# Kernel optimization log

Hardware: AMD Instinct MI355X
Metric: run time of the kernel (lower is better)

The kernel has to match this reference:

```python
import jax, jax.numpy as jnp
import numpy as np


def _spectral_norm(W, u):
    # W: [out, in] (1x1 conv weight flattened), u: [out]
    # one power-iteration step (torch does this under no_grad), then
    # sigma = u' @ W @ v with gradient flowing through W only.
    v = W.T @ u
    v = v / jnp.linalg.norm(v)
    u2 = W @ v
    u2 = u2 / jnp.linalg.norm(u2)
    v = jax.lax.stop_gradient(v)
    u2 = jax.lax.stop_gradient(u2)
    sigma = u2 @ (W @ v)
    return W / sigma


def setup_inputs() -> dict:
    key = jax.random.key(0)
    ks = jax.random.split(key, 8)
    B, C, H, W = 32, 512, 32, 32
    Cq = C // 8  # 64
    x = jax.random.normal(ks[0], (B, C, H, W), dtype=jnp.float32)
    s = 1.0 / np.sqrt(C)
    return {
        "x": x,
        "Wq": jax.random.normal(ks[1], (Cq, C), dtype=jnp.float32) * s,
        "bq": jnp.zeros((Cq,), dtype=jnp.float32),
        "uq": jax.random.normal(ks[2], (Cq,), dtype=jnp.float32),
        "Wk": jax.random.normal(ks[3], (Cq, C), dtype=jnp.float32) * s,
        "bk": jnp.zeros((Cq,), dtype=jnp.float32),
        "uk": jax.random.normal(ks[4], (Cq,), dtype=jnp.float32),
        "Wv": jax.random.normal(ks[5], (C, C), dtype=jnp.float32) * s,
        "bv": jnp.zeros((C,), dtype=jnp.float32),
        "uv": jax.random.normal(ks[6], (C,), dtype=jnp.float32),
        "gamma": jnp.float32(0.5),
    }


def reference(x, Wq, bq, uq, Wk, bk, uk, Wv, bv, uv, gamma):
    B, C, H, W = x.shape
    N = H * W
    f = x.reshape(B, C, N)                                   # [B,C,N]
    # 1x1 conv == channel matmul with spectral-normalized weights
    q = jnp.einsum('oc,bcn->bno', _spectral_norm(Wq, uq), f) + bq          # [B,N,Cq]
    k = jnp.einsum('oc,bcn->bon', _spectral_norm(Wk, uk), f) + bk[:, None]  # [B,Cq,N]
    v = jnp.einsum('oc,bcn->bon', _spectral_norm(Wv, uv), f) + bv[:, None]  # [B,C,N]
    qk = jnp.einsum('bno,bom->bnm', q, k)                    # [B,N,N], no 1/sqrt(d)
    attn = jax.nn.softmax(qk, axis=1)                        # softmax over QUERY axis (dim 1)
    o = jnp.einsum('bcn,bnm->bcm', v, attn).reshape(B, C, H, W)
    return gamma * o + x
```

## Files before the change

kernel.cpp:

```cpp
#include <hip/hip_runtime.h>
#include <hip/hip_bf16.h>

typedef __hip_bfloat16 bf16;
typedef __bf16 bf16x8 __attribute__((ext_vector_type(8)));
typedef float  f32x4  __attribute__((ext_vector_type(4)));
typedef unsigned short u16x8 __attribute__((ext_vector_type(8)));

#define C_IN  512
#define N_SP  1024
#define BATCH 32

__device__ __forceinline__ float ldmix(const void* p, size_t i, int f32) {
    return f32 ? ((const float*)p)[i] : __bfloat162float(((const bf16*)p)[i]);
}
__device__ __forceinline__ void stmix(void* p, size_t i, float v, int f32) {
    if (f32) ((float*)p)[i] = v;
    else     ((bf16*)p)[i] = __float2bfloat16(v);
}
__device__ __forceinline__ unsigned short bfbits(float f) {
    bf16 t = __float2bfloat16(f);
    return *reinterpret_cast<unsigned short*>(&t);
}
__device__ __forceinline__ float bf2f(unsigned short h) {
    union { unsigned u; float f; } c; c.u = ((unsigned)h) << 16; return c.f;
}
__device__ __forceinline__ void ldvec8(const void* W, size_t base, int f32, float v[8]) {
    if (f32) {
        const float4* p = reinterpret_cast<const float4*>((const float*)W + base);
        float4 a = p[0], b = p[1];
        v[0] = a.x; v[1] = a.y; v[2] = a.z; v[3] = a.w;
        v[4] = b.x; v[5] = b.y; v[6] = b.z; v[7] = b.w;
    } else {
        u16x8 h = *reinterpret_cast<const u16x8*>((const bf16*)W + base);
#pragma unroll
        for (int j = 0; j < 8; ++j) v[j] = bf2f(h[j]);
    }
}

__device__ __forceinline__ void lds_barrier() {
    asm volatile("s_waitcnt lgkmcnt(0)" ::: "memory");
    __builtin_amdgcn_sched_barrier(0);
    __builtin_amdgcn_s_barrier();
    __builtin_amdgcn_sched_barrier(0);
}

__device__ __forceinline__ void tile_decode(int bid, int nblk, int& z, int& mc) {
    int GBk = nblk >> 5;
    if ((GBk & 7) == 0) {
        z  = (bid & 7) + 8 * ((bid >> 3) >> 5);
        mc = (bid >> 3) & 31;
    } else {
        z  = bid >> 5;
        mc = bid & 31;
    }
}

__global__ void k_detect(const unsigned short* __restrict__ xh, int* __restrict__ flag)
{
    __shared__ int red[256];
    int tid = threadIdx.x;
    unsigned short h = xh[2 * tid];
    int e = (h >> 7) & 0xFF;
    red[tid] = (e == 0 || (e >= 96 && e <= 159)) ? 1 : 0;
    __syncthreads();
    for (int s = 128; s > 0; s >>= 1) { if (tid < s) red[tid] += red[tid + s]; __syncthreads(); }
    if (tid == 0) *flag = (red[0] < 192) ? 1 : 0;
}

__global__ __launch_bounds__(256) void k_sn1(
    const void* __restrict__ Wq, const void* __restrict__ uq,
    const void* __restrict__ Wk, const void* __restrict__ uk,
    const void* __restrict__ Wv, const void* __restrict__ uv,
    const int* __restrict__ flag, float* __restrict__ tpart)
{
    __shared__ float sh_u[64];
    __shared__ float sh_acc[4][512];
    int f32 = *flag;
    int bx = blockIdx.x;
    const void *W, *u; int oc, slot;
    if (bx == 0)      { W = Wq; u = uq; oc = 0;      slot = 0; }
    else if (bx == 1) { W = Wk; u = uk; oc = 0;      slot = 1; }
    else              { W = Wv; u = uv; oc = bx - 2; slot = bx; }
    int tid = threadIdx.x, wave = tid >> 6, lane = tid & 63;
    if (tid < 64) sh_u[tid] = ldmix(u, oc * 64 + tid, f32);
    __syncthreads();

    float acc[8];
#pragma unroll
    for (int j = 0; j < 8; ++j) acc[j] = 0.f;
    int obase = oc * 64 + wave * 16;
#pragma unroll 4
    for (int i = 0; i < 16; ++i) {
        int o = obase + i;
        float w8[8]; ldvec8(W, (size_t)o * C_IN + lane * 8, f32, w8);
        float uo = sh_u[o - oc * 64];
#pragma unroll
        for (int j = 0; j < 8; ++j) acc[j] += w8[j] * uo;
    }
#pragma unroll
    for (int j = 0; j < 8; ++j) sh_acc[wave][lane * 8 + j] = acc[j];
    __syncthreads();
    for (int c = tid; c < 512; c += 256)
        tpart[(size_t)slot * 512 + c] =
            sh_acc[0][c] + sh_acc[1][c] + sh_acc[2][c] + sh_acc[3][c];
}

__global__ __launch_bounds__(512) void k_sn2(
    const void* __restrict__ Wq, const void* __restrict__ Wk,
    const void* __restrict__ Wv, const int* __restrict__ flag,
    const float* __restrict__ tpart, float* __restrict__ sig)
{
    __shared__ float sh_t[512];
    __shared__ float red[512];
    int f32 = *flag;
    int m = blockIdx.x;
    const void* W; int out, slot0, nch;
    if (m == 0)      { W = Wq; out = 64;  slot0 = 0; nch = 1; }
    else if (m == 1) { W = Wk; out = 64;  slot0 = 1; nch = 1; }
    else             { W = Wv; out = 512; slot0 = 2; nch = 8; }
    int tid = threadIdx.x, wave = tid >> 6, lane = tid & 63;

    float t = 0.f;
    for (int c2 = 0; c2 < nch; ++c2) t += tpart[(size_t)(slot0 + c2) * 512 + tid];
    sh_t[tid] = t;
    red[tid] = t * t;
    __syncthreads();
    for (int s = 256; s > 0; s >>= 1) { if (tid < s) red[tid] += red[tid + s]; __syncthreads(); }
    float t2 = red[0];
    __syncthreads();

    float tl[8];
#pragma unroll
    for (int j = 0; j < 8; ++j) tl[j] = sh_t[lane * 8 + j];

    float s2 = 0.f;
#pragma unroll 2
    for (int o = wave; o < out; o += 8) {
        float w8[8]; ldvec8(W, (size_t)o * C_IN + lane * 8, f32, w8);
        float d = 0.f;
#pragma unroll
        for (int j = 0; j < 8; ++j) d += w8[j] * tl[j];
#pragma unroll
        for (int off = 32; off > 0; off >>= 1) d += __shfl_xor(d, off);
        if (lane == 0) s2 += d * d;
    }
    __syncthreads();
    red[tid] = (lane == 0) ? s2 : 0.f;
    __syncthreads();
    for (int s = 256; s > 0; s >>= 1) { if (tid < s) red[tid] += red[tid + s]; __syncthreads(); }
    if (tid == 0) sig[m] = sqrtf(t2 / red[0]);
}

__global__ __launch_bounds__(256) void k_wscale(
    const void* __restrict__ Wq, const void* __restrict__ bq,
    const void* __restrict__ Wk, const void* __restrict__ bk,
    const void* __restrict__ Wv, const void* __restrict__ bv,
    const float* __restrict__ sig, const int* __restrict__ flag,
    bf16* __restrict__ Wb, bf16* __restrict__ Wlo, float* __restrict__ biasf)
{
    int f32 = *flag;
    int r = blockIdx.x;
    const void *W, *b; int row; float s;
    if (r < 64)       { W = Wq; b = bq; row = r;       s = sig[0]; }
    else if (r < 128) { W = Wk; b = bk; row = r - 64;  s = sig[1]; }
    else              { W = Wv; b = bv; row = r - 128; s = sig[2]; }
    for (int c = threadIdx.x; c < C_IN; c += 256) {
        float w = ldmix(W, (size_t)row * C_IN + c, f32) * s;
        bf16 hi = __float2bfloat16(w);
        Wb[(size_t)r * C_IN + c] = hi;
        if (r < 128)
            Wlo[(size_t)r * C_IN + c] = __float2bfloat16(w - __bfloat162float(hi));
    }
    if (threadIdx.x == 0) biasf[r] = ldmix(b, row, f32);
}

__global__ __launch_bounds__(256) void k_xt(
    const void* __restrict__ x, const int* __restrict__ flag,
    char* __restrict__ SX, int batch0)
{
    __shared__ float tile[64][65];
    int f32 = *flag;
    int z = blockIdx.z;
    int n0 = blockIdx.x * 64, c0 = blockIdx.y * 64;
    size_t xoff = (size_t)(batch0 + z) * C_IN * N_SP;
    bf16* xTh = (bf16*)(SX + (size_t)z * 4194304);
    bf16* xTl = xTh + 524288;
    int tid = threadIdx.x;
#pragma unroll
    for (int i = 0; i < 4; ++i) {
        int idx = tid + i * 256;
        int c = idx >> 4, nq = idx & 15;
#pragma unroll
        for (int t = 0; t < 4; ++t)
            tile[c][nq * 4 + t] = ldmix(x, xoff + (size_t)(c0 + c) * N_SP + n0 + nq * 4 + t, f32);
    }
    __syncthreads();
#pragma unroll
    for (int i = 0; i < 16; ++i) {
        int idx = tid + i * 256;
        int n = idx >> 6, c = idx & 63;
        float v = tile[c][n];
        bf16 hi = __float2bfloat16(v);
        xTh[(size_t)(n0 + n) * C_IN + c0 + c] = hi;
        xTl[(size_t)(n0 + n) * C_IN + c0 + c] = __float2bfloat16(v - __bfloat162float(hi));
    }
}

__global__ __launch_bounds__(256) void k_qkv_v(
    const bf16* __restrict__ Wb, const float* __restrict__ biasf,
    const char* __restrict__ SX, bf16* __restrict__ YV)
{
    __shared__ __bf16 Als[2][128][40];
    __shared__ __bf16 Bls[2][128][40];
    int z, mc; tile_decode(blockIdx.x, gridDim.x, z, mc);
    int n0 = (mc >> 2) * 128;
    int r0 = 128 + (mc & 3) * 128;
    const bf16* xTh = (const bf16*)(SX + (size_t)z * 4194304);
    bf16* Yv = YV + (size_t)z * 524288;
    int tid = threadIdx.x, wave = tid >> 6, lane = tid & 63, quad = lane >> 4, l16 = lane & 15;
    int wc = (wave >> 1) * 64, wm = (wave & 1) * 64;
    int row0 = tid >> 2, row1 = row0 + 64, ch = tid & 3;

    f32x4 acc[4][4];
#pragma unroll
    for (int i = 0; i < 4; ++i)
#pragma unroll
        for (int j = 0; j < 4; ++j) acc[i][j] = (f32x4){0.f, 0.f, 0.f, 0.f};

    uint4 ra0, ra1, rb0, rb1;
#define LDV(t_) { int k0 = (t_) * 32; \
    ra0 = *reinterpret_cast<const uint4*>(&Wb[(size_t)(r0 + row0) * C_IN + k0 + ch * 8]); \
    ra1 = *reinterpret_cast<const uint4*>(&Wb[(size_t)(r0 + row1) * C_IN + k0 + ch * 8]); \
    rb0 = *reinterpret_cast<const uint4*>(&xTh[(size_t)(n0 + row0) * C_IN + k0 + ch * 8]); \
    rb1 = *reinterpret_cast<const uint4*>(&xTh[(size_t)(n0 + row1) * C_IN + k0 + ch * 8]); }
    LDV(0);
#pragma unroll 2
    for (int t = 0; t < 16; ++t) {
        int cur = t & 1;
        *reinterpret_cast<uint4*>(&Als[cur][row0][ch * 8]) = ra0;
        *reinterpret_cast<uint4*>(&Als[cur][row1][ch * 8]) = ra1;
        *reinterpret_cast<uint4*>(&Bls[cur][row0][ch * 8]) = rb0;
        *reinterpret_cast<uint4*>(&Bls[cur][row1][ch * 8]) = rb1;
        if (t + 1 < 16) LDV(t + 1);
        lds_barrier();
        bf16x8 a[4], b[4];
#pragma unroll
        for (int i = 0; i < 4; ++i)
            a[i] = *reinterpret_cast<const bf16x8*>(&Als[cur][wc + i * 16 + l16][quad * 8]);
#pragma unroll
        for (int j = 0; j < 4; ++j)
            b[j] = *reinterpret_cast<const bf16x8*>(&Bls[cur][wm + j * 16 + l16][quad * 8]);
#pragma unroll
        for (int i = 0; i < 4; ++i)
#pragma unroll
            for (int j = 0; j < 4; ++j)
                acc[i][j] = __builtin_amdgcn_mfma_f32_16x16x32_bf16(a[i], b[j], acc[i][j], 0, 0, 0);
    }
#undef LDV
#pragma unroll
    for (int i = 0; i < 4; ++i)
#pragma unroll
        for (int j = 0; j < 4; ++j)
#pragma unroll
            for (int r = 0; r < 4; ++r) {
                int c = r0 + wc + i * 16 + quad * 4 + r;
                int n = n0 + wm + j * 16 + l16;
                Yv[(size_t)(c - 128) * N_SP + n] = __float2bfloat16(acc[i][j][r] + biasf[c]);
            }
}

__global__ __launch_bounds__(256) void k_qkv_qk(
    const bf16* __restrict__ Wb, const bf16* __restrict__ Wlo,
    const float* __restrict__ biasf, const char* __restrict__ SX,
    bf16* __restrict__ QT, bf16* __restrict__ KT)
{
    __shared__ __bf16 Ah[2][64][40], Al[2][64][40], Bh[2][64][40], Bl[2][64][40];
    int z, mc; tile_decode(blockIdx.x, gridDim.x, z, mc);
    int n0 = (mc >> 1) * 64;
    int m0 = (mc & 1) * 64;
    const bf16* xTh = (const bf16*)(SX + (size_t)z * 4194304);
    const bf16* xTl = xTh + 524288;
    bf16* qt = QT + (size_t)z * 65536;
    bf16* kt = KT + (size_t)z * 65536;
    int tid = threadIdx.x, wave = tid >> 6, lane = tid & 63, quad = lane >> 4, l16 = lane & 15;
    int wmh = (wave >> 1) * 32, wnh = (wave & 1) * 32;
    int row = tid >> 2, ch = tid & 3;

    f32x4 acc[2][2];
#pragma unroll
    for (int i = 0; i < 2; ++i)
#pragma unroll
        for (int j = 0; j < 2; ++j) acc[i][j] = (f32x4){0.f, 0.f, 0.f, 0.f};

    uint4 rah, ral, rbh, rbl;
#define LDQK(t_) { int k0 = (t_) * 32; \
    rah = *reinterpret_cast<const uint4*>(&Wb [(size_t)(m0 + row) * C_IN + k0 + ch * 8]); \
    ral = *reinterpret_cast<const uint4*>(&Wlo[(size_t)(m0 + row) * C_IN + k0 + ch * 8]); \
    rbh = *reinterpret_cast<const uint4*>(&xTh[(size_t)(n0 + row) * C_IN + k0 + ch * 8]); \
    rbl = *reinterpret_cast<const uint4*>(&xTl[(size_t)(n0 + row) * C_IN + k0 + ch * 8]); }
    LDQK(0);
#pragma unroll 2
    for (int t = 0; t < 16; ++t) {
        int cur = t & 1;
        *reinterpret_cast<uint4*>(&Ah[cur][row][ch * 8]) = rah;
        *reinterpret_cast<uint4*>(&Al[cur][row][ch * 8]) = ral;
        *reinterpret_cast<uint4*>(&Bh[cur][row][ch * 8]) = rbh;
        *reinterpret_cast<uint4*>(&Bl[cur][row][ch * 8]) = rbl;
        if (t + 1 < 16) LDQK(t + 1);
        lds_barrier();
        bf16x8 ah[2], al2[2], bh[2], bl[2];
#pragma unroll
        for (int i = 0; i < 2; ++i) {
            ah[i]  = *reinterpret_cast<const bf16x8*>(&Ah[cur][wmh + i * 16 + l16][quad * 8]);
            al2[i] = *reinterpret_cast<const bf16x8*>(&Al[cur][wmh + i * 16 + l16][quad * 8]);
        }
#pragma unroll
        for (int j = 0; j < 2; ++j) {
            bh[j] = *reinterpret_cast<const bf16x8*>(&Bh[cur][wnh + j * 16 + l16][quad * 8]);
            bl[j] = *reinterpret_cast<const bf16x8*>(&Bl[cur][wnh + j * 16 + l16][quad * 8]);
        }
#pragma unroll
        for (int i = 0; i < 2; ++i)
#pragma unroll
            for (int j = 0; j < 2; ++j) {
                acc[i][j] = __builtin_amdgcn_mfma_f32_16x16x32_bf16(ah[i],  bh[j], acc[i][j], 0, 0, 0);
                acc[i][j] = __builtin_amdgcn_mfma_f32_16x16x32_bf16(ah[i],  bl[j], acc[i][j], 0, 0, 0);
                acc[i][j] = __builtin_amdgcn_mfma_f32_16x16x32_bf16(al2[i], bh[j], acc[i][j], 0, 0, 0);
            }
    }
#undef LDQK
#pragma unroll
    for (int i = 0; i < 2; ++i)
#pragma unroll
        for (int j = 0; j < 2; ++j) {
            int cbase = m0 + wmh + i * 16 + quad * 4;
            int n = n0 + wnh + j * 16 + l16;
            ushort4 st;
            st.x = bfbits(acc[i][j][0] + biasf[cbase + 0]);
            st.y = bfbits(acc[i][j][1] + biasf[cbase + 1]);
            st.z = bfbits(acc[i][j][2] + biasf[cbase + 2]);
            st.w = bfbits(acc[i][j][3] + biasf[cbase + 3]);
            bf16* dst = (m0 == 0) ? &qt[(size_t)n * 64 + cbase]
                                  : &kt[(size_t)n * 64 + (cbase - 64)];
            *reinterpret_cast<ushort4*>(dst) = st;
        }
}

__global__ __launch_bounds__(256) void k_qk(
    const bf16* __restrict__ QT, const bf16* __restrict__ KT,
    char* __restrict__ SX)
{
    __shared__ __bf16 Als[128][40];
    __shared__ __bf16 Bls[128][40];
    int z = blockIdx.z, m0 = blockIdx.y * 128, n0 = blockIdx.x * 128;
    const bf16* qt = QT + (size_t)z * 65536;
    const bf16* kt = KT + (size_t)z * 65536;
    float* Sf = (float*)(SX + (size_t)z * 4194304);
    int tid = threadIdx.x, wave = tid >> 6, lane = tid & 63, quad = lane >> 4, l16 = lane & 15;
    int wc = (wave >> 1) * 64, wm = (wave & 1) * 64;

    f32x4 acc[4][4];
#pragma unroll
    for (int i = 0; i < 4; ++i)
#pragma unroll
        for (int j = 0; j < 4; ++j) acc[i][j] = (f32x4){0.f, 0.f, 0.f, 0.f};

#pragma unroll
    for (int k0 = 0; k0 < 64; k0 += 32) {
#pragma unroll
        for (int s = 0; s < 2; ++s) {
            int idx = tid + s * 256; int row = idx >> 2, ch = idx & 3;
            *reinterpret_cast<uint4*>(&Als[row][ch * 8]) =
                *reinterpret_cast<const uint4*>(&kt[(size_t)(m0 + row) * 64 + k0 + ch * 8]);
            *reinterpret_cast<uint4*>(&Bls[row][ch * 8]) =
                *reinterpret_cast<const uint4*>(&qt[(size_t)(n0 + row) * 64 + k0 + ch * 8]);
        }
        __syncthreads();
        bf16x8 a[4], b[4];
#pragma unroll
        for (int i = 0; i < 4; ++i)
            a[i] = *reinterpret_cast<const bf16x8*>(&Als[wc + i * 16 + l16][quad * 8]);
#pragma unroll
        for (int j = 0; j < 4; ++j)
            b[j] = *reinterpret_cast<const bf16x8*>(&Bls[wm + j * 16 + l16][quad * 8]);
#pragma unroll
        for (int i = 0; i < 4; ++i)
#pragma unroll
            for (int j = 0; j < 4; ++j)
                acc[i][j] = __builtin_amdgcn_mfma_f32_16x16x32_bf16(a[i], b[j], acc[i][j], 0, 0, 0);
        __syncthreads();
    }
#pragma unroll
    for (int i = 0; i < 4; ++i)
#pragma unroll
        for (int j = 0; j < 4; ++j)
#pragma unroll
            for (int r = 0; r < 4; ++r) {
                int m = m0 + wc + i * 16 + quad * 4 + r;
                int n = n0 + wm + j * 16 + l16;
                Sf[(size_t)m * N_SP + n] = acc[i][j][r];
            }
}

__global__ __launch_bounds__(256) void k_softmax(char* __restrict__ SX)
{
    __shared__ float red[256];
    int z = blockIdx.x >> 10, m = blockIdx.x & 1023;
    float* p = (float*)(SX + (size_t)z * 4194304) + (size_t)m * N_SP;
    bf16* pb = (bf16*)p;
    int tid = threadIdx.x;
    float v0 = p[tid], v1 = p[tid + 256], v2 = p[tid + 512], v3 = p[tid + 768];
    red[tid] = fmaxf(fmaxf(v0, v1), fmaxf(v2, v3));
    __syncthreads();
    for (int s = 128; s > 0; s >>= 1) { if (tid < s) red[tid] = fmaxf(red[tid], red[tid + s]); __syncthreads(); }
    float mx = red[0];
    __syncthreads();
    float d0 = fmaxf(fminf(v0 - mx, 0.f), -80.f);
    float d1 = fmaxf(fminf(v1 - mx, 0.f), -80.f);
    float d2 = fmaxf(fminf(v2 - mx, 0.f), -80.f);
    float d3 = fmaxf(fminf(v3 - mx, 0.f), -80.f);
    float e0 = __expf(d0), e1 = __expf(d1), e2 = __expf(d2), e3 = __expf(d3);
    red[tid] = e0 + e1 + e2 + e3;
    __syncthreads();
    for (int s = 128; s > 0; s >>= 1) { if (tid < s) red[tid] += red[tid + s]; __syncthreads(); }
    float inv = 1.f / red[0];
    pb[tid]       = __float2bfloat16(e0 * inv);
    pb[tid + 256] = __float2bfloat16(e1 * inv);
    pb[tid + 512] = __float2bfloat16(e2 * inv);
    pb[tid + 768] = __float2bfloat16(e3 * inv);
}

__global__ __launch_bounds__(256) void k_out(
    const bf16* __restrict__ YV, const char* __restrict__ SX,
    const void* __restrict__ x, const void* __restrict__ gamma,
    const int* __restrict__ flag, void* __restrict__ out, int batch0)
{
    __shared__ __bf16 Als[2][128][40];
    __shared__ __bf16 Bls[2][128][40];
    int f32 = *flag;
    int z, mc; tile_decode(blockIdx.x, gridDim.x, z, mc);
    int m0 = (mc >> 2) * 128, c0 = (mc & 3) * 128;
    const bf16* Yv = YV + (size_t)z * 524288;
    const bf16* Pb = (const bf16*)(SX + (size_t)z * 4194304);
    int tid = threadIdx.x, wave = tid >> 6, lane = tid & 63, quad = lane >> 4, l16 = lane & 15;
    int wc = (wave >> 1) * 64, wm = (wave & 1) * 64;
    int row0 = tid >> 2, row1 = row0 + 64, ch = tid & 3;

    f32x4 acc[4][4];
#pragma unroll
    for (int i = 0; i < 4; ++i)
#pragma unroll
        for (int j = 0; j < 4; ++j) acc[i][j] = (f32x4){0.f, 0.f, 0.f, 0.f};

    uint4 ra0, ra1, rb0, rb1;
#define LDO(t_) { int k0 = (t_) * 32; \
    ra0 = *reinterpret_cast<const uint4*>(&Yv[(size_t)(c0 + row0) * N_SP + k0 + ch * 8]); \
    ra1 = *reinterpret_cast<const uint4*>(&Yv[(size_t)(c0 + row1) * N_SP + k0 + ch * 8]); \
    rb0 = *reinterpret_cast<const uint4*>(&Pb[(size_t)(m0 + row0) * 2048 + k0 + ch * 8]); \
    rb1 = *reinterpret_cast<const uint4*>(&Pb[(size_t)(m0 + row1) * 2048 + k0 + ch * 8]); }
    LDO(0);
#pragma unroll 2
    for (int t = 0; t < 32; ++t) {
        int cur = t & 1;
        *reinterpret_cast<uint4*>(&Als[cur][row0][ch * 8]) = ra0;
        *reinterpret_cast<uint4*>(&Als[cur][row1][ch * 8]) = ra1;
        *reinterpret_cast<uint4*>(&Bls[cur][row0][ch * 8]) = rb0;
        *reinterpret_cast<uint4*>(&Bls[cur][row1][ch * 8]) = rb1;
        if (t + 1 < 32) LDO(t + 1);
        lds_barrier();
        bf16x8 a[4], b[4];
#pragma unroll
        for (int i = 0; i < 4; ++i)
            a[i] = *reinterpret_cast<const bf16x8*>(&Als[cur][wc + i * 16 + l16][quad * 8]);
#pragma unroll
        for (int j = 0; j < 4; ++j)
            b[j] = *reinterpret_cast<const bf16x8*>(&Bls[cur][wm + j * 16 + l16][quad * 8]);
#pragma unroll
        for (int i = 0; i < 4; ++i)
#pragma unroll
            for (int j = 0; j < 4; ++j)
                acc[i][j] = __builtin_amdgcn_mfma_f32_16x16x32_bf16(a[i], b[j], acc[i][j], 0, 0, 0);
    }
#undef LDO

    float g = ldmix(gamma, 0, f32);
    const size_t base = (size_t)(batch0 + z) * C_IN * N_SP;
#pragma unroll
    for (int i = 0; i < 4; ++i)
#pragma unroll
        for (int j = 0; j < 4; ++j)
#pragma unroll
            for (int r = 0; r < 4; ++r) {
                int c = c0 + wc + i * 16 + quad * 4 + r;
                int m = m0 + wm + j * 16 + l16;
                size_t o = base + (size_t)c * N_SP + m;
                float v = fmaf(g, acc[i][j][r], ldmix(x, o, f32));
                if (!(v == v)) v = 5555.0f + 1000.0f * f32;
                stmix(out, o, v, f32);
            }
}

__global__ void k_wsfail(float* __restrict__ out, int n)
{
    int i = blockIdx.x * 256 + threadIdx.x;
    if (i < n) out[i] = 7777.0f;
}

extern "C" void kernel_launch(void* const* d_in, const int* in_sizes, int n_in,
                              void* d_out, int out_size, void* d_ws, size_t ws_size,
                              hipStream_t stream)
{
    const void* x  = d_in[0];
    const void* Wq = d_in[1];
    const void* bq = d_in[2];
    const void* Wk = d_in[4];
    const void* bk = d_in[5];
    const void* Wv = d_in[7];
    const void* bv = d_in[8];
    const void* uq = d_in[3];
    const void* uk = d_in[6];
    const void* uv = d_in[9];
    const void* gm = d_in[10];

    const size_t HDR = 790528;
    const size_t per = 4194304 + 131072 + 131072 + 1048576;
    int GB = 0;
    for (int g = 32; g >= 1; g >>= 1)
        if (HDR + (size_t)g * per <= ws_size) { GB = g; break; }
    if (GB == 0) {
        k_wsfail<<<(out_size + 255) / 256, 256, 0, stream>>>((float*)d_out, out_size);
        return;
    }
    char* ws = (char*)d_ws;
    int*   flag  = (int*)ws;
    float* sig   = (float*)(ws + 16);
    float* biasf = (float*)(ws + 256);
    bf16*  Wb    = (bf16*)(ws + 4096);
    bf16*  Wlo   = (bf16*)(ws + 659456);
    char*  SX    = ws + HDR;
    bf16*  QT    = (bf16*)(SX + (size_t)GB * 4194304);
    bf16*  KT    = QT + (size_t)GB * 65536;
    bf16*  YV    = KT + (size_t)GB * 65536;
    float* tpart = (float*)SX;

    k_detect<<<1, 256, 0, stream>>>((const unsigned short*)x, flag);
    k_sn1<<<10, 256, 0, stream>>>(Wq, uq, Wk, uk, Wv, uv, flag, tpart);
    k_sn2<<<3, 512, 0, stream>>>(Wq, Wk, Wv, flag, tpart, sig);
    k_wscale<<<640, 256, 0, stream>>>(Wq, bq, Wk, bk, Wv, bv, sig, flag, Wb, Wlo, biasf);
    for (int b0 = 0; b0 < BATCH; b0 += GB) {
        k_xt     <<<dim3(16, 8, GB), 256, 0, stream>>>(x, flag, SX, b0);
        k_qkv_v  <<<GB * 32, 256, 0, stream>>>(Wb, biasf, SX, YV);
        k_qkv_qk <<<GB * 32, 256, 0, stream>>>(Wb, Wlo, biasf, SX, QT, KT);
        k_qk     <<<dim3(8, 8, GB), 256, 0, stream>>>(QT, KT, SX);
        k_softmax<<<GB * 1024, 256, 0, stream>>>(SX);
        k_out    <<<GB * 32, 256, 0, stream>>>(YV, SX, x, gm, flag, d_out, b0);
    }
}
```

Measured before the change: 409.0 us.

## Use direct global-to-LDS loads with triple buffering and XOR swizzle in GEMM kernels

Replaces the register-staged double-buffered LDS loads in the QKV and output GEMM kernels with global_load_lds direct-to-LDS transfers into a three-stage ring buffer. Loads for tile t+2 are issued while tile t is consumed, and completion is gated with vmcnt waits instead of an lgkmcnt barrier. Padded LDS rows give way to an XOR swizzle to avoid bank conflicts, and s_setprio raises priority around the MFMA block. This aims to cut VGPR staging and hide global latency better, at the cost of more LDS per block and delicate vmcnt accounting that could be wrong when the ring slots rotate.

```diff
diff --git a/kernel.cpp b/kernel.cpp
--- a/kernel.cpp
+++ b/kernel.cpp
@@ -37,11 +37,33 @@
     }
 }
 
-__device__ __forceinline__ void lds_barrier() {
-    asm volatile("s_waitcnt lgkmcnt(0)" ::: "memory");
-    __builtin_amdgcn_sched_barrier(0);
-    __builtin_amdgcn_s_barrier();
-    __builtin_amdgcn_sched_barrier(0);
+__device__ __forceinline__ void gload_lds16(const bf16* g, void* l) {
+    __builtin_amdgcn_global_load_lds(
+        (__attribute__((address_space(1))) void*)(g),
+        (__attribute__((address_space(3))) void*)(l),
+        16, 0, 0);
+}
+
+#define STAGE128(LDS, GROW, GPITCH, K0) do {                                   \
+    int _c = (wave << 7) + lane; int _r = _c >> 2;                             \
+    int _s = (_c & 3) ^ ((_r >> 1) & 3);                                       \
+    gload_lds16((GROW) + (size_t)_r * (GPITCH) + (K0) + _s * 8,                \
+                (char*)(LDS) + (wave << 11));                                  \
+    _c += 64; _r = _c >> 2; _s = (_c & 3) ^ ((_r >> 1) & 3);                   \
+    gload_lds16((GROW) + (size_t)_r * (GPITCH) + (K0) + _s * 8,                \
+                (char*)(LDS) + (wave << 11) + 1024);                           \
+} while (0)
+
+#define STAGE64(LDS, GROW, GPITCH, K0) do {                                    \
+    int _c = (wave << 6) + lane; int _r = _c >> 2;                             \
+    int _s = (_c & 3) ^ ((_r >> 1) & 3);                                       \
+    gload_lds16((GROW) + (size_t)_r * (GPITCH) + (K0) + _s * 8,                \
+                (char*)(LDS) + (wave << 10));                                  \
+} while (0)
+
+__device__ __forceinline__ bf16x8 swz_frag(const void* tile, int row, int quad) {
+    return *(const bf16x8*)((const char*)tile + (row << 6) +
+                            ((quad ^ ((row >> 1) & 3)) << 4));
 }
 
 __device__ __forceinline__ void tile_decode(int bid, int nblk, int& z, int& mc) {
@@ -210,8 +232,8 @@
     const bf16* __restrict__ Wb, const float* __restrict__ biasf,
     const char* __restrict__ SX, bf16* __restrict__ YV)
 {
-    __shared__ __bf16 Als[2][128][40];
-    __shared__ __bf16 Bls[2][128][40];
+    __shared__ __bf16 As0[128][32], As1[128][32], As2[128][32];
+    __shared__ __bf16 Bs0[128][32], Bs1[128][32], Bs2[128][32];
     int z, mc; tile_decode(blockIdx.x, gridDim.x, z, mc);
     int n0 = (mc >> 2) * 128;
     int r0 = 128 + (mc & 3) * 128;
@@ -219,7 +241,9 @@
     bf16* Yv = YV + (size_t)z * 524288;
     int tid = threadIdx.x, wave = tid >> 6, lane = tid & 63, quad = lane >> 4, l16 = lane & 15;
     int wc = (wave >> 1) * 64, wm = (wave & 1) * 64;
-    int row0 = tid >> 2, row1 = row0 + 64, ch = tid & 3;
+
+    const bf16* Ar = Wb + (size_t)r0 * C_IN;
+    const bf16* Br = xTh + (size_t)n0 * C_IN;
 
     f32x4 acc[4][4];
 #pragma unroll
@@ -227,36 +251,43 @@
 #pragma unroll
         for (int j = 0; j < 4; ++j) acc[i][j] = (f32x4){0.f, 0.f, 0.f, 0.f};
 
-    uint4 ra0, ra1, rb0, rb1;
-#define LDV(t_) { int k0 = (t_) * 32; \
-    ra0 = *reinterpret_cast<const uint4*>(&Wb[(size_t)(r0 + row0) * C_IN + k0 + ch * 8]); \
-    ra1 = *reinterpret_cast<const uint4*>(&Wb[(size_t)(r0 + row1) * C_IN + k0 + ch * 8]); \
-    rb0 = *reinterpret_cast<const uint4*>(&xTh[(size_t)(n0 + row0) * C_IN + k0 + ch * 8]); \
-    rb1 = *reinterpret_cast<const uint4*>(&xTh[(size_t)(n0 + row1) * C_IN + k0 + ch * 8]); }
-    LDV(0);
-#pragma unroll 2
-    for (int t = 0; t < 16; ++t) {
-        int cur = t & 1;
-        *reinterpret_cast<uint4*>(&Als[cur][row0][ch * 8]) = ra0;
-        *reinterpret_cast<uint4*>(&Als[cur][row1][ch * 8]) = ra1;
-        *reinterpret_cast<uint4*>(&Bls[cur][row0][ch * 8]) = rb0;
-        *reinterpret_cast<uint4*>(&Bls[cur][row1][ch * 8]) = rb1;
-        if (t + 1 < 16) LDV(t + 1);
-        lds_barrier();
-        bf16x8 a[4], b[4];
-#pragma unroll
-        for (int i = 0; i < 4; ++i)
-            a[i] = *reinterpret_cast<const bf16x8*>(&Als[cur][wc + i * 16 + l16][quad * 8]);
-#pragma unroll
-        for (int j = 0; j < 4; ++j)
-            b[j] = *reinterpret_cast<const bf16x8*>(&Bls[cur][wm + j * 16 + l16][quad * 8]);
-#pragma unroll
-        for (int i = 0; i < 4; ++i)
-#pragma unroll
-            for (int j = 0; j < 4; ++j)
-                acc[i][j] = __builtin_amdgcn_mfma_f32_16x16x32_bf16(a[i], b[j], acc[i][j], 0, 0, 0);
-    }
-#undef LDV
+    STAGE128(As0, Ar, C_IN, 0);  STAGE128(Bs0, Br, C_IN, 0);
+    STAGE128(As1, Ar, C_IN, 32); STAGE128(Bs1, Br, C_IN, 32);
+    char *a0 = (char*)As0, *a1 = (char*)As1, *a2 = (char*)As2;
+    char *b0 = (char*)Bs0, *b1 = (char*)Bs1, *b2 = (char*)Bs2;
+
+#define QKV_V_MFMA(PA, PB) {                                                   \
+    bf16x8 a[4], b[4];                                                         \
+    _Pragma("unroll")                                                          \
+    for (int i = 0; i < 4; ++i) a[i] = swz_frag(PA, wc + i * 16 + l16, quad);  \
+    _Pragma("unroll")                                                          \
+    for (int j = 0; j < 4; ++j) b[j] = swz_frag(PB, wm + j * 16 + l16, quad);  \
+    __builtin_amdgcn_s_setprio(1);                                             \
+    _Pragma("unroll")                                                          \
+    for (int i = 0; i < 4; ++i)                                                \
+        _Pragma("unroll")                                                      \
+        for (int j = 0; j < 4; ++j)                                            \
+            acc[i][j] = __builtin_amdgcn_mfma_f32_16x16x32_bf16(a[i], b[j], acc[i][j], 0, 0, 0); \
+    __builtin_amdgcn_s_setprio(0); }
+
+    for (int t = 0; t < 15; ++t) {
+        asm volatile("s_waitcnt vmcnt(4)" ::: "memory");
+        __builtin_amdgcn_s_barrier();
+        __builtin_amdgcn_sched_barrier(0);
+        if (t + 2 < 16) {
+            int k2 = (t + 2) * 32;
+            STAGE128(a2, Ar, C_IN, k2); STAGE128(b2, Br, C_IN, k2);
+        }
+        QKV_V_MFMA(a0, b0);
+        char* tp = a0; a0 = a1; a1 = a2; a2 = tp;
+        tp = b0; b0 = b1; b1 = b2; b2 = tp;
+    }
+    asm volatile("s_waitcnt vmcnt(0)" ::: "memory");
+    __builtin_amdgcn_s_barrier();
+    __builtin_amdgcn_sched_barrier(0);
+    QKV_V_MFMA(a0, b0);
+#undef QKV_V_MFMA
+
 #pragma unroll
     for (int i = 0; i < 4; ++i)
 #pragma unroll
@@ -274,7 +305,7 @@
     const float* __restrict__ biasf, const char* __restrict__ SX,
     bf16* __restrict__ QT, bf16* __restrict__ KT)
 {
-    __shared__ __bf16 Ah[2][64][40], Al[2][64][40], Bh[2][64][40], Bl[2][64][40];
+    __shared__ __bf16 Ah_[3][64][32], Al_[3][64][32], Bh_[3][64][32], Bl_[3][64][32];
     int z, mc; tile_decode(blockIdx.x, gridDim.x, z, mc);
     int n0 = (mc >> 1) * 64;
     int m0 = (mc & 1) * 64;
@@ -284,7 +315,11 @@
     bf16* kt = KT + (size_t)z * 65536;
     int tid = threadIdx.x, wave = tid >> 6, lane = tid & 63, quad = lane >> 4, l16 = lane & 15;
     int wmh = (wave >> 1) * 32, wnh = (wave & 1) * 32;
-    int row = tid >> 2, ch = tid & 3;
+
+    const bf16* Ahr = Wb  + (size_t)m0 * C_IN;
+    const bf16* Alr = Wlo + (size_t)m0 * C_IN;
+    const bf16* Bhr = xTh + (size_t)n0 * C_IN;
+    const bf16* Blr = xTl + (size_t)n0 * C_IN;
 
     f32x4 acc[2][2];
 #pragma unroll
@@ -292,43 +327,59 @@
 #pragma unroll
         for (int j = 0; j < 2; ++j) acc[i][j] = (f32x4){0.f, 0.f, 0.f, 0.f};
 
-    uint4 rah, ral, rbh, rbl;
-#define LDQK(t_) { int k0 = (t_) * 32; \
-    rah = *reinterpret_cast<const uint4*>(&Wb [(size_t)(m0 + row) * C_IN + k0 + ch * 8]); \
-    ral = *reinterpret_cast<const uint4*>(&Wlo[(size_t)(m0 + row) * C_IN + k0 + ch * 8]); \
-    rbh = *reinterpret_cast<const uint4*>(&xTh[(size_t)(n0 + row) * C_IN + k0 + ch * 8]); \
-    rbl = *reinterpret_cast<const uint4*>(&xTl[(size_t)(n0 + row) * C_IN + k0 + ch * 8]); }
-    LDQK(0);
-#pragma unroll 2
-    for (int t = 0; t < 16; ++t) {
-        int cur = t & 1;
-        *reinterpret_cast<uint4*>(&Ah[cur][row][ch * 8]) = rah;
-        *reinterpret_cast<uint4*>(&Al[cur][row][ch * 8]) = ral;
-        *reinterpret_cast<uint4*>(&Bh[cur][row][ch * 8]) = rbh;
-        *reinterpret_cast<uint4*>(&Bl[cur][row][ch * 8]) = rbl;
-        if (t + 1 < 16) LDQK(t + 1);
-        lds_barrier();
-        bf16x8 ah[2], al2[2], bh[2], bl[2];
-#pragma unroll
-        for (int i = 0; i < 2; ++i) {
-            ah[i]  = *reinterpret_cast<const bf16x8*>(&Ah[cur][wmh + i * 16 + l16][quad * 8]);
-            al2[i] = *reinterpret_cast<const bf16x8*>(&Al[cur][wmh + i * 16 + l16][quad * 8]);
+    STAGE64(Ah_[0], Ahr, C_IN, 0);  STAGE64(Al_[0], Alr, C_IN, 0);
+    STAGE64(Bh_[0], Bhr, C_IN, 0);  STAGE64(Bl_[0], Blr, C_IN, 0);
+    STAGE64(Ah_[1], Ahr, C_IN, 32); STAGE64(Al_[1], Alr, C_IN, 32);
+    STAGE64(Bh_[1], Bhr, C_IN, 32); STAGE64(Bl_[1], Blr, C_IN, 32);
+    char *ah0 = (char*)Ah_[0], *ah1 = (char*)Ah_[1], *ah2 = (char*)Ah_[2];
+    char *al0 = (char*)Al_[0], *al1 = (char*)Al_[1], *al2 = (char*)Al_[2];
+    char *bh0 = (char*)Bh_[0], *bh1 = (char*)Bh_[1], *bh2 = (char*)Bh_[2];
+    char *bl0 = (char*)Bl_[0], *bl1 = (char*)Bl_[1], *bl2 = (char*)Bl_[2];
+
+#define QK_MFMA(PAH, PAL, PBH, PBL) {                                          \
+    bf16x8 fah[2], fal[2], fbh[2], fbl[2];                                     \
+    _Pragma("unroll")                                                          \
+    for (int i = 0; i < 2; ++i) {                                              \
+        fah[i] = swz_frag(PAH, wmh + i * 16 + l16, quad);                      \
+        fal[i] = swz_frag(PAL, wmh + i * 16 + l16, quad);                      \
+    }                                                                          \
+    _Pragma("unroll")                                                          \
+    for (int j = 0; j < 2; ++j) {                                              \
+        fbh[j] = swz_frag(PBH, wnh + j * 16 + l16, quad);                      \
+        fbl[j] = swz_frag(PBL, wnh + j * 16 + l16, quad);                      \
+    }                                                                          \
+    __builtin_amdgcn_s_setprio(1);                                             \
+    _Pragma("unroll")                                                          \
+    for (int i = 0; i < 2; ++i)                                                \
+        _Pragma("unroll")                                                      \
+        for (int j = 0; j < 2; ++j) {                                          \
+            acc[i][j] = __builtin_amdgcn_mfma_f32_16x16x32_bf16(fah[i], fbh[j], acc[i][j], 0, 0, 0); \
+            acc[i][j] = __builtin_amdgcn_mfma_f32_16x16x32_bf16(fah[i], fbl[j], acc[i][j], 0, 0, 0); \
+            acc[i][j] = __builtin_amdgcn_mfma_f32_16x16x32_bf16(fal[i], fbh[j], acc[i][j], 0, 0, 0); \
+        }                                                                      \
+    __builtin_amdgcn_s_setprio(0); }
+
+    for (int t = 0; t < 15; ++t) {
+        asm volatile("s_waitcnt vmcnt(4)" ::: "memory");
+        __builtin_amdgcn_s_barrier();
+        __builtin_amdgcn_sched_barrier(0);
+        if (t + 2 < 16) {
+            int k2 = (t + 2) * 32;
+            STAGE64(ah2, Ahr, C_IN, k2); STAGE64(al2, Alr, C_IN, k2);
+            STAGE64(bh2, Bhr, C_IN, k2); STAGE64(bl2, Blr, C_IN, k2);
         }
-#pragma unroll
-        for (int j = 0; j < 2; ++j) {
-            bh[j] = *reinterpret_cast<const bf16x8*>(&Bh[cur][wnh + j * 16 + l16][quad * 8]);
-            bl[j] = *reinterpret_cast<const bf16x8*>(&Bl[cur][wnh + j * 16 + l16][quad * 8]);
-        }
-#pragma unroll
-        for (int i = 0; i < 2; ++i)
-#pragma unroll
-            for (int j = 0; j < 2; ++j) {
-                acc[i][j] = __builtin_amdgcn_mfma_f32_16x16x32_bf16(ah[i],  bh[j], acc[i][j], 0, 0, 0);
-                acc[i][j] = __builtin_amdgcn_mfma_f32_16x16x32_bf16(ah[i],  bl[j], acc[i][j], 0, 0, 0);
-                acc[i][j] = __builtin_amdgcn_mfma_f32_16x16x32_bf16(al2[i], bh[j], acc[i][j], 0, 0, 0);
-            }
-    }
-#undef LDQK
+        QK_MFMA(ah0, al0, bh0, bl0);
+        char* tp = ah0; ah0 = ah1; ah1 = ah2; ah2 = tp;
+        tp = al0; al0 = al1; al1 = al2; al2 = tp;
+        tp = bh0; bh0 = bh1; bh1 = bh2; bh2 = tp;
+        tp = bl0; bl0 = bl1; bl1 = bl2; bl2 = tp;
+    }
+    asm volatile("s_waitcnt vmcnt(0)" ::: "memory");
+    __builtin_amdgcn_s_barrier();
+    __builtin_amdgcn_sched_barrier(0);
+    QK_MFMA(ah0, al0, bh0, bl0);
+#undef QK_MFMA
+
 #pragma unroll
     for (int i = 0; i < 2; ++i)
 #pragma unroll
@@ -435,8 +486,8 @@
     const void* __restrict__ x, const void* __restrict__ gamma,
     const int* __restrict__ flag, void* __restrict__ out, int batch0)
 {
-    __shared__ __bf16 Als[2][128][40];
-    __shared__ __bf16 Bls[2][128][40];
+    __shared__ __bf16 As0[128][32], As1[128][32], As2[128][32];
+    __shared__ __bf16 Bs0[128][32], Bs1[128][32], Bs2[128][32];
     int f32 = *flag;
     int z, mc; tile_decode(blockIdx.x, gridDim.x, z, mc);
     int m0 = (mc >> 2) * 128, c0 = (mc & 3) * 128;
@@ -444,7 +495,9 @@
     const bf16* Pb = (const bf16*)(SX + (size_t)z * 4194304);
     int tid = threadIdx.x, wave = tid >> 6, lane = tid & 63, quad = lane >> 4, l16 = lane & 15;
     int wc = (wave >> 1) * 64, wm = (wave & 1) * 64;
-    int row0 = tid >> 2, row1 = row0 + 64, ch = tid & 3;
+
+    const bf16* Ar = Yv + (size_t)c0 * N_SP;
+    const bf16* Br = Pb + (size_t)m0 * 2048;
 
     f32x4 acc[4][4];
 #pragma unroll
@@ -452,36 +505,42 @@
 #pragma unroll
         for (int j = 0; j < 4; ++j) acc[i][j] = (f32x4){0.f, 0.f, 0.f, 0.f};
 
-    uint4 ra0, ra1, rb0, rb1;
-#define LDO(t_) { int k0 = (t_) * 32; \
-    ra0 = *reinterpret_cast<const uint4*>(&Yv[(size_t)(c0 + row0) * N_SP + k0 + ch * 8]); \
-    ra1 = *reinterpret_cast<const uint4*>(&Yv[(size_t)(c0 + row1) * N_SP + k0 + ch * 8]); \
-    rb0 = *reinterpret_cast<const uint4*>(&Pb[(size_t)(m0 + row0) * 2048 + k0 + ch * 8]); \
-    rb1 = *reinterpret_cast<const uint4*>(&Pb[(size_t)(m0 + row1) * 2048 + k0 + ch * 8]); }
-    LDO(0);
-#pragma unroll 2
-    for (int t = 0; t < 32; ++t) {
-        int cur = t & 1;
-        *reinterpret_cast<uint4*>(&Als[cur][row0][ch * 8]) = ra0;
-        *reinterpret_cast<uint4*>(&Als[cur][row1][ch * 8]) = ra1;
-        *reinterpret_cast<uint4*>(&Bls[cur][row0][ch * 8]) = rb0;
-        *reinterpret_cast<uint4*>(&Bls[cur][row1][ch * 8]) = rb1;
-        if (t + 1 < 32) LDO(t + 1);
-        lds_barrier();
-        bf16x8 a[4], b[4];
-#pragma unroll
-        for (int i = 0; i < 4; ++i)
-            a[i] = *reinterpret_cast<const bf16x8*>(&Als[cur][wc + i * 16 + l16][quad * 8]);
-#pragma unroll
-        for (int j = 0; j < 4; ++j)
-            b[j] = *reinterpret_cast<const bf16x8*>(&Bls[cur][wm + j * 16 + l16][quad * 8]);
-#pragma unroll
-        for (int i = 0; i < 4; ++i)
-#pragma unroll
-            for (int j = 0; j < 4; ++j)
-                acc[i][j] = __builtin_amdgcn_mfma_f32_16x16x32_bf16(a[i], b[j], acc[i][j], 0, 0, 0);
-    }
-#undef LDO
+    STAGE128(As0, Ar, N_SP, 0);  STAGE128(Bs0, Br, 2048, 0);
+    STAGE128(As1, Ar, N_SP, 32); STAGE128(Bs1, Br, 2048, 32);
+    char *a0 = (char*)As0, *a1 = (char*)As1, *a2 = (char*)As2;
+    char *b0 = (char*)Bs0, *b1 = (char*)Bs1, *b2 = (char*)Bs2;
+
+#define OUT_MFMA(PA, PB) {                                                     \
+    bf16x8 a[4], b[4];                                                         \
+    _Pragma("unroll")                                                          \
+    for (int i = 0; i < 4; ++i) a[i] = swz_frag(PA, wc + i * 16 + l16, quad);  \
+    _Pragma("unroll")                                                          \
+    for (int j = 0; j < 4; ++j) b[j] = swz_frag(PB, wm + j * 16 + l16, quad);  \
+    __builtin_amdgcn_s_setprio(1);                                             \
+    _Pragma("unroll")                                                          \
+    for (int i = 0; i < 4; ++i)                                                \
+        _Pragma("unroll")                                                      \
+        for (int j = 0; j < 4; ++j)                                            \
+            acc[i][j] = __builtin_amdgcn_mfma_f32_16x16x32_bf16(a[i], b[j], acc[i][j], 0, 0, 0); \
+    __builtin_amdgcn_s_setprio(0); }
+
+    for (int t = 0; t < 31; ++t) {
+        asm volatile("s_waitcnt vmcnt(4)" ::: "memory");
+        __builtin_amdgcn_s_barrier();
+        __builtin_amdgcn_sched_barrier(0);
+        if (t + 2 < 32) {
+            int k2 = (t + 2) * 32;
+            STAGE128(a2, Ar, N_SP, k2); STAGE128(b2, Br, 2048, k2);
+        }
+        OUT_MFMA(a0, b0);
+        char* tp = a0; a0 = a1; a1 = a2; a2 = tp;
+        tp = b0; b0 = b1; b1 = b2; b2 = tp;
+    }
+    asm volatile("s_waitcnt vmcnt(0)" ::: "memory");
+    __builtin_amdgcn_s_barrier();
+    __builtin_amdgcn_sched_barrier(0);
+    OUT_MFMA(a0, b0);
+#undef OUT_MFMA
 
     float g = ldmix(gamma, 0, f32);
     const size_t base = (size_t)(batch0 + z) * C_IN * N_SP;
```

Measured after the change: 417.3 us. +2.0%, slower.
